# Kernel optimization log

Measured on AMD Instinct MI355X. Metric: run time of the kernel, lower is better.

The kernel has to match this reference:

```python
import jax, jax.numpy as jnp
import numpy as np

N_NODES = 100000
HID = 128
N_LAYERS = 3
N_EDGES = 1600000
EPS = 1e-5


def setup_inputs() -> dict:
    key = jax.random.key(0)
    ks = jax.random.split(key, 10)
    H, L = HID, N_LAYERS
    # edge_index: row 0 = src, row 1 = dst (PyG source_to_target flow)
    edge_index = jax.random.randint(ks[0], (2, N_EDGES), 0, N_NODES, dtype=jnp.int32)
    # xavier-uniform embedding
    lim = float(np.sqrt(6.0 / (N_NODES + H)))
    emb = jax.random.uniform(ks[1], (N_NODES, H), jnp.float32, -lim, lim)
    s = 1.0 / np.sqrt(H)
    Wl = jax.random.uniform(ks[2], (L, H, H), jnp.float32, -s, s)  # lin_l (neighbors), has bias
    bl = jax.random.uniform(ks[3], (L, H), jnp.float32, -s, s)
    Wr = jax.random.uniform(ks[4], (L, H, H), jnp.float32, -s, s)  # lin_r (root), no bias
    ln_gamma = jnp.ones((L, H), jnp.float32)
    ln_beta = jnp.zeros((L, H), jnp.float32)
    sj = 1.0 / np.sqrt(H * (L + 1))
    jkW = jax.random.uniform(ks[5], (H, H * (L + 1)), jnp.float32, -sj, sj)
    jkb = jax.random.uniform(ks[6], (H,), jnp.float32, -sj, sj)
    return {"emb": emb, "Wl": Wl, "bl": bl, "Wr": Wr,
            "ln_gamma": ln_gamma, "ln_beta": ln_beta,
            "jkW": jkW, "jkb": jkb, "edge_index": edge_index}


def _layernorm(x, gamma, beta):
    mu = jnp.mean(x, axis=-1, keepdims=True)
    var = jnp.mean(jnp.square(x - mu), axis=-1, keepdims=True)
    return (x - mu) * jax.lax.rsqrt(var + EPS) * gamma + beta


def reference(emb, Wl, bl, Wr, ln_gamma, ln_beta, jkW, jkb, edge_index):
    src, dst = edge_index[0], edge_index[1]
    n = emb.shape[0]
    # in-degree for mean aggregation (clamped to avoid div-by-zero)
    deg = jax.ops.segment_sum(jnp.ones_like(dst, dtype=emb.dtype), dst, num_segments=n)
    inv_deg = (1.0 / jnp.maximum(deg, 1.0))[:, None]
    x = emb
    xs = [x]
    for i in range(N_LAYERS):
        x_prev = x
        # scatter-mean of neighbor features (gather [E,H] -> segment_sum [N,H])
        agg = jax.ops.segment_sum(x[src], dst, num_segments=n) * inv_deg
        # SAGEConv: lin_l(agg) + lin_r(x)
        x = agg @ Wl[i].T + bl[i] + x @ Wr[i].T
        x = _layernorm(x, ln_gamma[i], ln_beta[i])
        x = jax.nn.relu(x)
        # dropout is identity in eval mode
        if i > 0:
            x = x + x_prev
        xs.append(x)
    # jumping-knowledge concat + projection
    x = jnp.concatenate(xs, axis=1) @ jkW.T + jkb
    return x
```

## Files before the change

kernel.cpp:

```cpp
#include <hip/hip_runtime.h>
#include <hip/hip_bf16.h>
#include <stdint.h>

#define HID 128
#define BSHIFT 7
#define NBLK 64

typedef __attribute__((ext_vector_type(8))) __bf16 bf16x8;
typedef __attribute__((ext_vector_type(4))) float f32x4;

static __device__ __forceinline__ float bf2f(ushort h){
  union { uint u; float f; } c; c.u = ((uint)h) << 16; return c.f;
}
static __device__ __forceinline__ ushort f2bf(float f){
  union { float f; uint u; } c; c.f = f;
  uint u = c.u;
  return (ushort)((u + 0x7fffu + ((u >> 16) & 1u)) >> 16);
}
static __device__ __forceinline__ bf16x8 load8(const ushort* p){
  return *(const bf16x8*)p;
}

__global__ void k_cvt(const float* __restrict__ in, ushort* __restrict__ out, int n){
  int i = blockIdx.x * 256 + threadIdx.x;
  if (i < n) out[i] = f2bf(in[i]);
}

__global__ void k_cvtw(const float* __restrict__ Wl, const float* __restrict__ Wr,
                       ushort* __restrict__ outF, int total){
  int o = blockIdx.x * 256 + threadIdx.x;
  if (o >= total) return;
  int layer = o >> 15;
  int r = o & 32767;
  int e    = r & 7;
  int lane = (r >> 3) & 63;
  int jt   = (r >> 9) & 7;
  int mat  = (r >> 12) & 1;
  int kt   = r >> 13;
  int l16 = lane & 15, quad = lane >> 4;
  int j = jt * 16 + l16;
  int k = kt * 32 + quad * 8 + e;
  const float* W = mat ? Wr : Wl;
  outF[o] = f2bf(W[layer * 16384 + j * 128 + k]);
}

__global__ void k_cvtjk(const float* __restrict__ jkW, ushort* __restrict__ outF){
  int o = blockIdx.x * 256 + threadIdx.x;
  int e    = o & 7;
  int lane = (o >> 3) & 63;
  int jt   = (o >> 9) & 7;
  int kt   = o >> 12;
  int l16 = lane & 15, quad = lane >> 4;
  int j = jt * 16 + l16;
  int k = kt * 32 + quad * 8 + e;
  outF[o] = f2bf(jkW[j * 512 + k]);
}

__global__ __launch_bounds__(1024) void k_count(
    const int* __restrict__ dst, int* __restrict__ rowcnt, int E, int NB, int es){
  __shared__ int h[1024];
  int blk = blockIdx.x;
  for (int i = threadIdx.x; i < NB; i += 1024) h[i] = 0;
  __syncthreads();
  int e0 = blk * es, e1 = min(e0 + es, E);
  for (int e = e0 + threadIdx.x; e < e1; e += 1024)
    atomicAdd(&h[dst[e] >> BSHIFT], 1);
  __syncthreads();
  for (int i = threadIdx.x; i < NB; i += 1024)
    rowcnt[blk * NB + i] = h[i];
}

__global__ __launch_bounds__(1024) void k_colscan(
    int* __restrict__ rowcnt, int* __restrict__ bbase, int NB, int nblk){
  int b = threadIdx.x;
  int total = 0;
  if (b < NB)
    for (int r = 0; r < nblk; r++) total += rowcnt[r * NB + b];
  int lane = b & 63, w = b >> 6;
  int x = total;
  #pragma unroll
  for (int d = 1; d < 64; d <<= 1){ int y = __shfl_up(x, d, 64); if (lane >= d) x += y; }
  __shared__ int tmp[16];
  if (lane == 63) tmp[w] = x;
  __syncthreads();
  if (b < 64){
    int s = (lane < 16) ? tmp[lane] : 0;
    #pragma unroll
    for (int d = 1; d < 16; d <<= 1){ int y = __shfl_up(s, d, 64); if (lane >= d) s += y; }
    if (lane < 16) tmp[lane] = s;
  }
  __syncthreads();
  int base = ((w > 0) ? tmp[w - 1] : 0) + x - total;
  if (b < NB){
    bbase[b] = base;
    int acc = base;
    for (int r = 0; r < nblk; r++){
      int v = rowcnt[r * NB + b];
      rowcnt[r * NB + b] = acc;
      acc += v;
    }
    if (b == NB - 1) bbase[NB] = acc;
  }
}

__global__ __launch_bounds__(1024) void k_place(
    const int* __restrict__ src, const int* __restrict__ dst,
    const int* __restrict__ rowcnt, uint* __restrict__ binned, int E, int NB, int es){
  __shared__ int cur[1024];
  int blk = blockIdx.x;
  for (int i = threadIdx.x; i < NB; i += 1024) cur[i] = rowcnt[blk * NB + i];
  __syncthreads();
  int e0 = blk * es, e1 = min(e0 + es, E);
  for (int e = e0 + threadIdx.x; e < e1; e += 1024){
    int d = dst[e];
    int b = d >> BSHIFT;
    int pos = atomicAdd(&cur[b], 1);
    binned[pos] = ((uint)src[e] << BSHIFT) | (uint)(d & 127);
  }
}

__global__ __launch_bounds__(256) void k_bpass(
    const uint* __restrict__ binned, const int* __restrict__ bbase,
    int* __restrict__ csr, int* __restrict__ offs, int* __restrict__ cnt, int N){
  int b = blockIdx.x;
  int n0 = b << BSHIFT;
  int tid = threadIdx.x;
  __shared__ int lcnt[128], loffs[128];
  if (tid < 128) lcnt[tid] = 0;
  __syncthreads();
  int base = bbase[b];
  int m = bbase[b + 1] - base;
  const uint* bp = binned + base;
  uint vv[12]; int slot[12];
  #pragma unroll
  for (int u = 0; u < 12; u++){
    int i = tid + u * 256;
    if (i < m){
      uint v = bp[i];
      vv[u] = v;
      slot[u] = atomicAdd(&lcnt[v & 127], 1);
    }
  }
  __syncthreads();
  if (tid < 64){
    int a0 = lcnt[tid * 2], a1 = lcnt[tid * 2 + 1];
    int s = a0 + a1;
    int x = s;
    #pragma unroll
    for (int d = 1; d < 64; d <<= 1){ int y = __shfl_up(x, d, 64); if (tid >= d) x += y; }
    int excl = x - s;
    loffs[tid * 2] = excl;
    loffs[tid * 2 + 1] = excl + a0;
  }
  __syncthreads();
  if (tid < 128 && n0 + tid < N){
    cnt[n0 + tid] = lcnt[tid];
    offs[n0 + tid] = base + loffs[tid];
  }
  #pragma unroll
  for (int u = 0; u < 12; u++){
    int i = tid + u * 256;
    if (i < m){
      uint v = vv[u];
      csr[base + loffs[v & 127] + slot[u]] = (int)(v >> BSHIFT);
    }
  }
}

__global__ __launch_bounds__(256) void k_aggregate(
    const ushort* __restrict__ x, const int* __restrict__ csr,
    const int* __restrict__ offs, const int* __restrict__ cnt,
    ushort* __restrict__ agg, int N){
  int node = blockIdx.x * 4 + (threadIdx.x >> 6);
  int lane = threadIdx.x & 63;
  if (node >= N) return;
  int half = lane >> 5;
  int l32  = lane & 31;
  int beg = offs[node], d = cnt[node];
  if (d == 0){
    if (half == 0){
      uint2 z = {0u, 0u};
      *(uint2*)(agg + (size_t)node * HID + l32 * 4) = z;
    }
    return;
  }
  const int* __restrict__ cp = csr + beg;
  float s0 = 0.f, s1 = 0.f, s2 = 0.f, s3 = 0.f;
  for (int i = 0; i < d; i += 16){
    int idx[8]; float w[8];
    #pragma unroll
    for (int u = 0; u < 8; u++){
      int pos = i + 2 * u + half;
      bool ok = pos < d;
      pos = ok ? pos : d - 1;
      idx[u] = cp[pos];
      w[u] = ok ? 1.f : 0.f;
    }
    uint2 v[8];
    #pragma unroll
    for (int u = 0; u < 8; u++)
      v[u] = *(const uint2*)(x + (size_t)idx[u] * HID + l32 * 4);
    #pragma unroll
    for (int u = 0; u < 8; u++){
      s0 = fmaf(w[u], bf2f((ushort)v[u].x), s0);
      s1 = fmaf(w[u], bf2f((ushort)(v[u].x >> 16)), s1);
      s2 = fmaf(w[u], bf2f((ushort)v[u].y), s2);
      s3 = fmaf(w[u], bf2f((ushort)(v[u].y >> 16)), s3);
    }
  }
  s0 += __shfl_xor(s0, 32, 64);
  s1 += __shfl_xor(s1, 32, 64);
  s2 += __shfl_xor(s2, 32, 64);
  s3 += __shfl_xor(s3, 32, 64);
  if (half == 0){
    float inv = 1.0f / fmaxf((float)d, 1.0f);
    uint2 o;
    o.x = (uint)f2bf(s0 * inv) | ((uint)f2bf(s1 * inv) << 16);
    o.y = (uint)f2bf(s2 * inv) | ((uint)f2bf(s3 * inv) << 16);
    *(uint2*)(agg + (size_t)node * HID + l32 * 4) = o;
  }
}

template<int HAS_RES>
__global__ __launch_bounds__(256) void k_layer(
    const ushort* __restrict__ agg, const ushort* __restrict__ xin,
    const ushort* __restrict__ Wf,
    const float* __restrict__ bl, const float* __restrict__ gamma,
    const float* __restrict__ beta,
    ushort* __restrict__ xout, int N){
  __shared__ ushort sB[8192];
  int tid = threadIdx.x;
  int wv = tid >> 6, lane = tid & 63;
  int quad = lane >> 4, l16 = lane & 15;
  int rowbase = blockIdx.x * 128 + wv * 32;
  int r0 = rowbase + l16;      if (r0 >= N) r0 = N - 1;
  int r1 = rowbase + 16 + l16; if (r1 >= N) r1 = N - 1;

  f32x4 acc[2][8];
  #pragma unroll
  for (int jt = 0; jt < 8; jt++){
    float b = bl[jt * 16 + l16];
    f32x4 c = {b, b, b, b};
    acc[0][jt] = c; acc[1][jt] = c;
  }

  #pragma unroll
  for (int kt = 0; kt < 4; kt++){
    int ao = kt * 32 + quad * 8;
    bf16x8 a10 = load8(agg + (size_t)r0 * HID + ao);
    bf16x8 a11 = load8(agg + (size_t)r1 * HID + ao);
    bf16x8 a20 = load8(xin + (size_t)r0 * HID + ao);
    bf16x8 a21 = load8(xin + (size_t)r1 * HID + ao);
    __syncthreads();
    const ushort* src = Wf + kt * 8192;
    #pragma unroll
    for (int i = 0; i < 4; i++){
      int c = i * 256 + tid;
      *(bf16x8*)(sB + c * 8) = load8(src + c * 8);
    }
    __syncthreads();
    #pragma unroll
    for (int jt = 0; jt < 8; jt++){
      bf16x8 bL = load8(sB + (jt * 64 + lane) * 8);
      bf16x8 bR = load8(sB + ((8 + jt) * 64 + lane) * 8);
      acc[0][jt] = __builtin_amdgcn_mfma_f32_16x16x32_bf16(a10, bL, acc[0][jt], 0, 0, 0);
      acc[1][jt] = __builtin_amdgcn_mfma_f32_16x16x32_bf16(a11, bL, acc[1][jt], 0, 0, 0);
      acc[0][jt] = __builtin_amdgcn_mfma_f32_16x16x32_bf16(a20, bR, acc[0][jt], 0, 0, 0);
      acc[1][jt] = __builtin_amdgcn_mfma_f32_16x16x32_bf16(a21, bR, acc[1][jt], 0, 0, 0);
    }
  }

  #pragma unroll
  for (int rt = 0; rt < 2; rt++){
    float s1[4] = {0,0,0,0}, s2[4] = {0,0,0,0};
    #pragma unroll
    for (int jt = 0; jt < 8; jt++){
      #pragma unroll
      for (int r = 0; r < 4; r++){ float v = acc[rt][jt][r]; s1[r] += v; s2[r] += v * v; }
    }
    #pragma unroll
    for (int m = 1; m < 16; m <<= 1){
      #pragma unroll
      for (int r = 0; r < 4; r++){
        s1[r] += __shfl_xor(s1[r], m, 64);
        s2[r] += __shfl_xor(s2[r], m, 64);
      }
    }
    float mu[4], rs[4];
    #pragma unroll
    for (int r = 0; r < 4; r++){
      mu[r] = s1[r] * (1.f / 128.f);
      float var = s2[r] * (1.f / 128.f) - mu[r] * mu[r];
      rs[r] = rsqrtf(var + 1e-5f);
    }
    #pragma unroll
    for (int jt = 0; jt < 8; jt++){
      int col = jt * 16 + l16;
      float g = gamma[col], bb = beta[col];
      #pragma unroll
      for (int r = 0; r < 4; r++){
        int row = rowbase + rt * 16 + quad * 4 + r;
        if (row < N){
          float v = (acc[rt][jt][r] - mu[r]) * rs[r] * g + bb;
          v = fmaxf(v, 0.f);
          if (HAS_RES) v += bf2f(xin[(size_t)row * HID + col]);
          xout[(size_t)row * HID + col] = f2bf(v);
        }
      }
    }
  }
}

__global__ __launch_bounds__(256) void k_jk(
    const ushort* __restrict__ emb, const ushort* __restrict__ x1,
    const ushort* __restrict__ x2, const ushort* __restrict__ x3,
    const ushort* __restrict__ Wf,
    const float* __restrict__ jkb, float* __restrict__ out, int N){
  __shared__ ushort sB[8192];
  int tid = threadIdx.x;
  int wv = tid >> 6, lane = tid & 63;
  int quad = lane >> 4, l16 = lane & 15;
  int rowbase = blockIdx.x * 128 + wv * 32;
  int r0 = rowbase + l16;      if (r0 >= N) r0 = N - 1;
  int r1 = rowbase + 16 + l16; if (r1 >= N) r1 = N - 1;

  f32x4 acc[2][8];
  #pragma unroll
  for (int jt = 0; jt < 8; jt++){
    float b = jkb[jt * 16 + l16];
    f32x4 c = {b, b, b, b};
    acc[0][jt] = c; acc[1][jt] = c;
  }

  const ushort* srcs[4] = {emb, x1, x2, x3};
  #pragma unroll
  for (int st = 0; st < 8; st++){
    int kt0 = st * 2, kt1 = st * 2 + 1;
    const ushort* sp0 = srcs[kt0 >> 2];
    const ushort* sp1 = srcs[kt1 >> 2];
    int ao0 = (kt0 & 3) * 32 + quad * 8;
    int ao1 = (kt1 & 3) * 32 + quad * 8;
    bf16x8 aA0 = load8(sp0 + (size_t)r0 * HID + ao0);
    bf16x8 aA1 = load8(sp0 + (size_t)r1 * HID + ao0);
    bf16x8 aB0 = load8(sp1 + (size_t)r0 * HID + ao1);
    bf16x8 aB1 = load8(sp1 + (size_t)r1 * HID + ao1);
    __syncthreads();
    const ushort* src = Wf + st * 8192;
    #pragma unroll
    for (int i = 0; i < 4; i++){
      int c = i * 256 + tid;
      *(bf16x8*)(sB + c * 8) = load8(src + c * 8);
    }
    __syncthreads();
    #pragma unroll
    for (int jt = 0; jt < 8; jt++){
      bf16x8 b0 = load8(sB + (jt * 64 + lane) * 8);
      bf16x8 b1 = load8(sB + ((8 + jt) * 64 + lane) * 8);
      acc[0][jt] = __builtin_amdgcn_mfma_f32_16x16x32_bf16(aA0, b0, acc[0][jt], 0, 0, 0);
      acc[1][jt] = __builtin_amdgcn_mfma_f32_16x16x32_bf16(aA1, b0, acc[1][jt], 0, 0, 0);
      acc[0][jt] = __builtin_amdgcn_mfma_f32_16x16x32_bf16(aB0, b1, acc[0][jt], 0, 0, 0);
      acc[1][jt] = __builtin_amdgcn_mfma_f32_16x16x32_bf16(aB1, b1, acc[1][jt], 0, 0, 0);
    }
  }

  #pragma unroll
  for (int rt = 0; rt < 2; rt++){
    #pragma unroll
    for (int jt = 0; jt < 8; jt++){
      #pragma unroll
      for (int r = 0; r < 4; r++){
        int row = rowbase + rt * 16 + quad * 4 + r;
        if (row < N)
          out[(size_t)row * HID + jt * 16 + l16] = acc[rt][jt][r];
      }
    }
  }
}

extern "C" void kernel_launch(void* const* d_in, const int* in_sizes, int n_in,
                              void* d_out, int out_size, void* d_ws, size_t ws_size,
                              hipStream_t stream){
  const float* emb   = (const float*)d_in[0];
  const float* Wl    = (const float*)d_in[1];
  const float* bl    = (const float*)d_in[2];
  const float* Wr    = (const float*)d_in[3];
  const float* gamma = (const float*)d_in[4];
  const float* beta  = (const float*)d_in[5];
  const float* jkW   = (const float*)d_in[6];
  const float* jkb   = (const float*)d_in[7];
  const int*   eidx  = (const int*)d_in[8];
  int N = in_sizes[0] / HID;
  int E = in_sizes[8] / 2;
  const int* src = eidx;
  const int* dst = eidx + E;
  float* out = (float*)d_out;

  int NB = (N + 127) >> BSHIFT;
  int es = (E + NBLK - 1) / NBLK;

  char* w = (char*)d_ws;
  auto carve = [&](size_t bytes) -> char* {
    char* p = w; w += (bytes + 255) & ~(size_t)255; return p;
  };
  int Npad = ((N + 127) / 128) * 128;
  int* rowcnt   = (int*)carve((size_t)NBLK * NB * 4);
  int* bbase    = (int*)carve((size_t)(NB + 1) * 4);
  uint* binned  = (uint*)carve((size_t)E * 4);
  int* cnt      = (int*)carve((size_t)N * 4);
  int* offs     = (int*)carve((size_t)N * 4);
  int* csr      = (int*)carve((size_t)E * 4);
  ushort* Wfrag = (ushort*)carve((size_t)3 * 32768 * 2);
  ushort* jkWf  = (ushort*)carve((size_t)65536 * 2);
  ushort* embbf = (ushort*)carve((size_t)Npad * HID * 2);
  ushort* agg   = (ushort*)carve((size_t)Npad * HID * 2);
  ushort* x1    = (ushort*)carve((size_t)Npad * HID * 2);
  ushort* x2    = (ushort*)carve((size_t)Npad * HID * 2);
  ushort* x3    = (ushort*)carve((size_t)Npad * HID * 2);

  int nEmb = N * HID;
  k_cvtw<<<(3 * 32768 + 255) / 256, 256, 0, stream>>>(Wl, Wr, Wfrag, 3 * 32768);
  k_cvtjk<<<65536 / 256, 256, 0, stream>>>(jkW, jkWf);
  k_cvt<<<(nEmb + 255) / 256, 256, 0, stream>>>(emb, embbf, nEmb);

  k_count<<<NBLK, 1024, 0, stream>>>(dst, rowcnt, E, NB, es);
  k_colscan<<<1, 1024, 0, stream>>>(rowcnt, bbase, NB, NBLK);
  k_place<<<NBLK, 1024, 0, stream>>>(src, dst, rowcnt, binned, E, NB, es);
  k_bpass<<<NB, 256, 0, stream>>>(binned, bbase, csr, offs, cnt, N);

  int aggBlocks = (N + 3) / 4;
  int gemmBlocks = (N + 127) / 128;

  k_aggregate<<<aggBlocks, 256, 0, stream>>>(embbf, csr, offs, cnt, agg, N);
  k_layer<0><<<gemmBlocks, 256, 0, stream>>>(agg, embbf, Wfrag, bl, gamma, beta, x1, N);
  k_aggregate<<<aggBlocks, 256, 0, stream>>>(x1, csr, offs, cnt, agg, N);
  k_layer<1><<<gemmBlocks, 256, 0, stream>>>(agg, x1, Wfrag + 32768, bl + HID,
                                             gamma + HID, beta + HID, x2, N);
  k_aggregate<<<aggBlocks, 256, 0, stream>>>(x2, csr, offs, cnt, agg, N);
  k_layer<1><<<gemmBlocks, 256, 0, stream>>>(agg, x2, Wfrag + 2 * 32768, bl + 2 * HID,
                                             gamma + 2 * HID, beta + 2 * HID, x3, N);
  k_jk<<<gemmBlocks, 256, 0, stream>>>(embbf, x1, x2, x3, jkWf, jkb, out, N);
}
```

Before: 555.9 us.

## Persistent GEMM blocks with weights resident in LDS; fast path in aggregation

The layer and JK GEMM kernels become persistent: a grid of at most 512 blocks loops over row tiles. In k_layer the full 64 KB weight matrix is loaded into LDS once per block, removing the per-tile weight reloads and most barriers. k_jk loads two 64 KB weight halves per tile, so it still reloads weights but with fewer syncs. The aggregation loop gains an unmasked fast path for full 16-edge chunks and keeps the masked path only for the tail. The larger LDS footprint limits occupancy to about two blocks per CU.

```diff
diff --git a/kernel.cpp b/kernel.cpp
--- a/kernel.cpp
+++ b/kernel.cpp
@@ -186,7 +186,24 @@
   }
   const int* __restrict__ cp = csr + beg;
   float s0 = 0.f, s1 = 0.f, s2 = 0.f, s3 = 0.f;
-  for (int i = 0; i < d; i += 16){
+  int i = 0;
+  for (; i + 16 <= d; i += 16){
+    int idx[8];
+    #pragma unroll
+    for (int u = 0; u < 8; u++) idx[u] = cp[i + 2 * u + half];
+    uint2 v[8];
+    #pragma unroll
+    for (int u = 0; u < 8; u++)
+      v[u] = *(const uint2*)(x + (size_t)idx[u] * HID + l32 * 4);
+    #pragma unroll
+    for (int u = 0; u < 8; u++){
+      s0 += bf2f((ushort)v[u].x);
+      s1 += bf2f((ushort)(v[u].x >> 16));
+      s2 += bf2f((ushort)v[u].y);
+      s3 += bf2f((ushort)(v[u].y >> 16));
+    }
+  }
+  if (i < d){
     int idx[8]; float w[8];
     #pragma unroll
     for (int u = 0; u < 8; u++){
@@ -222,156 +239,170 @@
 }
 
 template<int HAS_RES>
-__global__ __launch_bounds__(256) void k_layer(
+__global__ __launch_bounds__(256, 2) void k_layer(
     const ushort* __restrict__ agg, const ushort* __restrict__ xin,
     const ushort* __restrict__ Wf,
     const float* __restrict__ bl, const float* __restrict__ gamma,
     const float* __restrict__ beta,
-    ushort* __restrict__ xout, int N){
-  __shared__ ushort sB[8192];
+    ushort* __restrict__ xout, int N, int nTiles){
+  __shared__ ushort sB[32768];
   int tid = threadIdx.x;
   int wv = tid >> 6, lane = tid & 63;
   int quad = lane >> 4, l16 = lane & 15;
-  int rowbase = blockIdx.x * 128 + wv * 32;
-  int r0 = rowbase + l16;      if (r0 >= N) r0 = N - 1;
-  int r1 = rowbase + 16 + l16; if (r1 >= N) r1 = N - 1;
-
-  f32x4 acc[2][8];
+
   #pragma unroll
-  for (int jt = 0; jt < 8; jt++){
-    float b = bl[jt * 16 + l16];
-    f32x4 c = {b, b, b, b};
-    acc[0][jt] = c; acc[1][jt] = c;
-  }
-
-  #pragma unroll
-  for (int kt = 0; kt < 4; kt++){
-    int ao = kt * 32 + quad * 8;
-    bf16x8 a10 = load8(agg + (size_t)r0 * HID + ao);
-    bf16x8 a11 = load8(agg + (size_t)r1 * HID + ao);
-    bf16x8 a20 = load8(xin + (size_t)r0 * HID + ao);
-    bf16x8 a21 = load8(xin + (size_t)r1 * HID + ao);
-    __syncthreads();
-    const ushort* src = Wf + kt * 8192;
-    #pragma unroll
-    for (int i = 0; i < 4; i++){
-      int c = i * 256 + tid;
-      *(bf16x8*)(sB + c * 8) = load8(src + c * 8);
-    }
-    __syncthreads();
+  for (int i = 0; i < 16; i++){
+    int c = i * 256 + tid;
+    *(bf16x8*)(sB + c * 8) = load8(Wf + c * 8);
+  }
+  __syncthreads();
+
+  for (int tile = blockIdx.x; tile < nTiles; tile += gridDim.x){
+    int rowbase = tile * 128 + wv * 32;
+    int r0 = rowbase + l16;      if (r0 >= N) r0 = N - 1;
+    int r1 = rowbase + 16 + l16; if (r1 >= N) r1 = N - 1;
+
+    bf16x8 aL0[4], aL1[4], aR0[4], aR1[4];
+    #pragma unroll
+    for (int kt = 0; kt < 4; kt++){
+      int ao = kt * 32 + quad * 8;
+      aL0[kt] = load8(agg + (size_t)r0 * HID + ao);
+      aL1[kt] = load8(agg + (size_t)r1 * HID + ao);
+      aR0[kt] = load8(xin + (size_t)r0 * HID + ao);
+      aR1[kt] = load8(xin + (size_t)r1 * HID + ao);
+    }
+
+    f32x4 acc[2][8];
     #pragma unroll
     for (int jt = 0; jt < 8; jt++){
-      bf16x8 bL = load8(sB + (jt * 64 + lane) * 8);
-      bf16x8 bR = load8(sB + ((8 + jt) * 64 + lane) * 8);
-      acc[0][jt] = __builtin_amdgcn_mfma_f32_16x16x32_bf16(a10, bL, acc[0][jt], 0, 0, 0);
-      acc[1][jt] = __builtin_amdgcn_mfma_f32_16x16x32_bf16(a11, bL, acc[1][jt], 0, 0, 0);
-      acc[0][jt] = __builtin_amdgcn_mfma_f32_16x16x32_bf16(a20, bR, acc[0][jt], 0, 0, 0);
-      acc[1][jt] = __builtin_amdgcn_mfma_f32_16x16x32_bf16(a21, bR, acc[1][jt], 0, 0, 0);
-    }
-  }
-
-  #pragma unroll
-  for (int rt = 0; rt < 2; rt++){
-    float s1[4] = {0,0,0,0}, s2[4] = {0,0,0,0};
-    #pragma unroll
-    for (int jt = 0; jt < 8; jt++){
-      #pragma unroll
-      for (int r = 0; r < 4; r++){ float v = acc[rt][jt][r]; s1[r] += v; s2[r] += v * v; }
-    }
-    #pragma unroll
-    for (int m = 1; m < 16; m <<= 1){
+      float b = bl[jt * 16 + l16];
+      f32x4 c = {b, b, b, b};
+      acc[0][jt] = c; acc[1][jt] = c;
+    }
+
+    #pragma unroll
+    for (int kt = 0; kt < 4; kt++){
+      #pragma unroll
+      for (int jt = 0; jt < 8; jt++){
+        bf16x8 bL = load8(sB + ((kt * 16 + jt) * 64 + lane) * 8);
+        bf16x8 bR = load8(sB + ((kt * 16 + 8 + jt) * 64 + lane) * 8);
+        acc[0][jt] = __builtin_amdgcn_mfma_f32_16x16x32_bf16(aL0[kt], bL, acc[0][jt], 0, 0, 0);
+        acc[1][jt] = __builtin_amdgcn_mfma_f32_16x16x32_bf16(aL1[kt], bL, acc[1][jt], 0, 0, 0);
+        acc[0][jt] = __builtin_amdgcn_mfma_f32_16x16x32_bf16(aR0[kt], bR, acc[0][jt], 0, 0, 0);
+        acc[1][jt] = __builtin_amdgcn_mfma_f32_16x16x32_bf16(aR1[kt], bR, acc[1][jt], 0, 0, 0);
+      }
+    }
+
+    #pragma unroll
+    for (int rt = 0; rt < 2; rt++){
+      float s1[4] = {0,0,0,0}, s2[4] = {0,0,0,0};
+      #pragma unroll
+      for (int jt = 0; jt < 8; jt++){
+        #pragma unroll
+        for (int r = 0; r < 4; r++){ float v = acc[rt][jt][r]; s1[r] += v; s2[r] += v * v; }
+      }
+      #pragma unroll
+      for (int m = 1; m < 16; m <<= 1){
+        #pragma unroll
+        for (int r = 0; r < 4; r++){
+          s1[r] += __shfl_xor(s1[r], m, 64);
+          s2[r] += __shfl_xor(s2[r], m, 64);
+        }
+      }
+      float mu[4], rs[4];
       #pragma unroll
       for (int r = 0; r < 4; r++){
-        s1[r] += __shfl_xor(s1[r], m, 64);
-        s2[r] += __shfl_xor(s2[r], m, 64);
-      }
-    }
-    float mu[4], rs[4];
-    #pragma unroll
-    for (int r = 0; r < 4; r++){
-      mu[r] = s1[r] * (1.f / 128.f);
-      float var = s2[r] * (1.f / 128.f) - mu[r] * mu[r];
-      rs[r] = rsqrtf(var + 1e-5f);
-    }
-    #pragma unroll
-    for (int jt = 0; jt < 8; jt++){
-      int col = jt * 16 + l16;
-      float g = gamma[col], bb = beta[col];
-      #pragma unroll
-      for (int r = 0; r < 4; r++){
-        int row = rowbase + rt * 16 + quad * 4 + r;
-        if (row < N){
-          float v = (acc[rt][jt][r] - mu[r]) * rs[r] * g + bb;
-          v = fmaxf(v, 0.f);
-          if (HAS_RES) v += bf2f(xin[(size_t)row * HID + col]);
-          xout[(size_t)row * HID + col] = f2bf(v);
+        mu[r] = s1[r] * (1.f / 128.f);
+        float var = s2[r] * (1.f / 128.f) - mu[r] * mu[r];
+        rs[r] = rsqrtf(var + 1e-5f);
+      }
+      #pragma unroll
+      for (int jt = 0; jt < 8; jt++){
+        int col = jt * 16 + l16;
+        float g = gamma[col], bb = beta[col];
+        #pragma unroll
+        for (int r = 0; r < 4; r++){
+          int row = rowbase + rt * 16 + quad * 4 + r;
+          if (row < N){
+            float v = (acc[rt][jt][r] - mu[r]) * rs[r] * g + bb;
+            v = fmaxf(v, 0.f);
+            if (HAS_RES) v += bf2f(xin[(size_t)row * HID + col]);
+            xout[(size_t)row * HID + col] = f2bf(v);
+          }
         }
       }
     }
   }
 }
 
-__global__ __launch_bounds__(256) void k_jk(
+__global__ __launch_bounds__(256, 2) void k_jk(
     const ushort* __restrict__ emb, const ushort* __restrict__ x1,
     const ushort* __restrict__ x2, const ushort* __restrict__ x3,
     const ushort* __restrict__ Wf,
-    const float* __restrict__ jkb, float* __restrict__ out, int N){
-  __shared__ ushort sB[8192];
+    const float* __restrict__ jkb, float* __restrict__ out, int N, int nTiles){
+  __shared__ ushort sB[32768];
   int tid = threadIdx.x;
   int wv = tid >> 6, lane = tid & 63;
   int quad = lane >> 4, l16 = lane & 15;
-  int rowbase = blockIdx.x * 128 + wv * 32;
-  int r0 = rowbase + l16;      if (r0 >= N) r0 = N - 1;
-  int r1 = rowbase + 16 + l16; if (r1 >= N) r1 = N - 1;
-
-  f32x4 acc[2][8];
-  #pragma unroll
-  for (int jt = 0; jt < 8; jt++){
-    float b = jkb[jt * 16 + l16];
-    f32x4 c = {b, b, b, b};
-    acc[0][jt] = c; acc[1][jt] = c;
-  }
-
-  const ushort* srcs[4] = {emb, x1, x2, x3};
-  #pragma unroll
-  for (int st = 0; st < 8; st++){
-    int kt0 = st * 2, kt1 = st * 2 + 1;
-    const ushort* sp0 = srcs[kt0 >> 2];
-    const ushort* sp1 = srcs[kt1 >> 2];
-    int ao0 = (kt0 & 3) * 32 + quad * 8;
-    int ao1 = (kt1 & 3) * 32 + quad * 8;
-    bf16x8 aA0 = load8(sp0 + (size_t)r0 * HID + ao0);
-    bf16x8 aA1 = load8(sp0 + (size_t)r1 * HID + ao0);
-    bf16x8 aB0 = load8(sp1 + (size_t)r0 * HID + ao1);
-    bf16x8 aB1 = load8(sp1 + (size_t)r1 * HID + ao1);
-    __syncthreads();
-    const ushort* src = Wf + st * 8192;
-    #pragma unroll
-    for (int i = 0; i < 4; i++){
-      int c = i * 256 + tid;
-      *(bf16x8*)(sB + c * 8) = load8(src + c * 8);
-    }
-    __syncthreads();
+
+  for (int tile = blockIdx.x; tile < nTiles; tile += gridDim.x){
+    int rowbase = tile * 128 + wv * 32;
+    int r0 = rowbase + l16;      if (r0 >= N) r0 = N - 1;
+    int r1 = rowbase + 16 + l16; if (r1 >= N) r1 = N - 1;
+
+    f32x4 acc[2][8];
     #pragma unroll
     for (int jt = 0; jt < 8; jt++){
-      bf16x8 b0 = load8(sB + (jt * 64 + lane) * 8);
-      bf16x8 b1 = load8(sB + ((8 + jt) * 64 + lane) * 8);
-      acc[0][jt] = __builtin_amdgcn_mfma_f32_16x16x32_bf16(aA0, b0, acc[0][jt], 0, 0, 0);
-      acc[1][jt] = __builtin_amdgcn_mfma_f32_16x16x32_bf16(aA1, b0, acc[1][jt], 0, 0, 0);
-      acc[0][jt] = __builtin_amdgcn_mfma_f32_16x16x32_bf16(aB0, b1, acc[0][jt], 0, 0, 0);
-      acc[1][jt] = __builtin_amdgcn_mfma_f32_16x16x32_bf16(aB1, b1, acc[1][jt], 0, 0, 0);
-    }
-  }
-
-  #pragma unroll
-  for (int rt = 0; rt < 2; rt++){
-    #pragma unroll
-    for (int jt = 0; jt < 8; jt++){
-      #pragma unroll
-      for (int r = 0; r < 4; r++){
-        int row = rowbase + rt * 16 + quad * 4 + r;
-        if (row < N)
-          out[(size_t)row * HID + jt * 16 + l16] = acc[rt][jt][r];
+      float b = jkb[jt * 16 + l16];
+      f32x4 c = {b, b, b, b};
+      acc[0][jt] = c; acc[1][jt] = c;
+    }
+
+    #pragma unroll
+    for (int h = 0; h < 2; h++){
+      const ushort* sA = h ? x2 : emb;
+      const ushort* sC = h ? x3 : x1;
+      bf16x8 aA0[4], aA1[4], aC0[4], aC1[4];
+      #pragma unroll
+      for (int kt = 0; kt < 4; kt++){
+        int ao = kt * 32 + quad * 8;
+        aA0[kt] = load8(sA + (size_t)r0 * HID + ao);
+        aA1[kt] = load8(sA + (size_t)r1 * HID + ao);
+        aC0[kt] = load8(sC + (size_t)r0 * HID + ao);
+        aC1[kt] = load8(sC + (size_t)r1 * HID + ao);
+      }
+      __syncthreads();
+      const ushort* src = Wf + h * 32768;
+      #pragma unroll
+      for (int i = 0; i < 16; i++){
+        int c = i * 256 + tid;
+        *(bf16x8*)(sB + c * 8) = load8(src + c * 8);
+      }
+      __syncthreads();
+      #pragma unroll
+      for (int kt = 0; kt < 4; kt++){
+        #pragma unroll
+        for (int jt = 0; jt < 8; jt++){
+          bf16x8 bA = load8(sB + ((kt * 8 + jt) * 64 + lane) * 8);
+          bf16x8 bC = load8(sB + (((4 + kt) * 8 + jt) * 64 + lane) * 8);
+          acc[0][jt] = __builtin_amdgcn_mfma_f32_16x16x32_bf16(aA0[kt], bA, acc[0][jt], 0, 0, 0);
+          acc[1][jt] = __builtin_amdgcn_mfma_f32_16x16x32_bf16(aA1[kt], bA, acc[1][jt], 0, 0, 0);
+          acc[0][jt] = __builtin_amdgcn_mfma_f32_16x16x32_bf16(aC0[kt], bC, acc[0][jt], 0, 0, 0);
+          acc[1][jt] = __builtin_amdgcn_mfma_f32_16x16x32_bf16(aC1[kt], bC, acc[1][jt], 0, 0, 0);
+        }
+      }
+    }
+
+    #pragma unroll
+    for (int rt = 0; rt < 2; rt++){
+      #pragma unroll
+      for (int jt = 0; jt < 8; jt++){
+        #pragma unroll
+        for (int r = 0; r < 4; r++){
+          int row = rowbase + rt * 16 + quad * 4 + r;
+          if (row < N)
+            out[(size_t)row * HID + jt * 16 + l16] = acc[rt][jt][r];
+        }
       }
     }
   }
@@ -428,15 +459,16 @@
   k_bpass<<<NB, 256, 0, stream>>>(binned, bbase, csr, offs, cnt, N);
 
   int aggBlocks = (N + 3) / 4;
-  int gemmBlocks = (N + 127) / 128;
+  int nTiles = (N + 127) / 128;
+  int gemmGrid = nTiles < 512 ? nTiles : 512;
 
   k_aggregate<<<aggBlocks, 256, 0, stream>>>(embbf, csr, offs, cnt, agg, N);
-  k_layer<0><<<gemmBlocks, 256, 0, stream>>>(agg, embbf, Wfrag, bl, gamma, beta, x1, N);
+  k_layer<0><<<gemmGrid, 256, 0, stream>>>(agg, embbf, Wfrag, bl, gamma, beta, x1, N, nTiles);
   k_aggregate<<<aggBlocks, 256, 0, stream>>>(x1, csr, offs, cnt, agg, N);
-  k_layer<1><<<gemmBlocks, 256, 0, stream>>>(agg, x1, Wfrag + 32768, bl + HID,
-                                             gamma + HID, beta + HID, x2, N);
+  k_layer<1><<<gemmGrid, 256, 0, stream>>>(agg, x1, Wfrag + 32768, bl + HID,
+                                           gamma + HID, beta + HID, x2, N, nTiles);
   k_aggregate<<<aggBlocks, 256, 0, stream>>>(x2, csr, offs, cnt, agg, N);
-  k_layer<1><<<gemmBlocks, 256, 0, stream>>>(agg, x2, Wfrag + 2 * 32768, bl + 2 * HID,
-                                             gamma + 2 * HID, beta + 2 * HID, x3, N);
-  k_jk<<<gemmBlocks, 256, 0, stream>>>(embbf, x1, x2, x3, jkWf, jkb, out, N);
-}
+  k_layer<1><<<gemmGrid, 256, 0, stream>>>(agg, x2, Wfrag + 2 * 32768, bl + 2 * HID,
+                                           gamma + 2 * HID, beta + 2 * HID, x3, N, nTiles);
+  k_jk<<<gemmGrid, 256, 0, stream>>>(embbf, x1, x2, x3, jkWf, jkb, out, N, nTiles);
+}
```

Measured after the change: 665.1 us. +19.6%, slower.
